# Performance work log

Measured on AMD Instinct MI355X. Metric: run time of the kernel, lower is better.

## Reference

```python
import jax, jax.numpy as jnp
import numpy as np
jax.config.update("jax_enable_x64", True)

T_OLD = 60000
T_NEW = 60000
NV = 30000
MAX_STEPS = 300
FB_CHUNK = 500  # T_OLD must be divisible by this

FACE_OPP = np.array([[1, 2, 3], [0, 2, 3], [0, 1, 3], [0, 1, 2]])
EDGES = [(0, 1), (0, 2), (0, 3), (1, 2), (1, 3), (2, 3)]


def setup_inputs() -> dict:
    key = jax.random.key(0)
    k1, k2, k3, k4, k5 = jax.random.split(key, 5)
    # distinct vertices per tet (sorted base + strictly increasing offsets)
    off = jnp.arange(4, dtype=jnp.int64)
    new_indices = jnp.sort(jax.random.randint(k1, (T_NEW, 4), 0, NV - 4, dtype=jnp.int64), axis=1) + off
    old_indices = jnp.sort(jax.random.randint(k2, (T_OLD, 4), 0, NV - 4, dtype=jnp.int64), axis=1) + off
    return {
        "new_indices": new_indices,
        "old_indices": old_indices,
        "old_cc": jax.random.normal(k3, (T_OLD, 3), dtype=jnp.float32),
        "new_cc": jax.random.normal(k4, (T_NEW, 3), dtype=jnp.float32),
        "vertex_positions": jax.random.uniform(k5, (NV, 3), dtype=jnp.float32),
    }


def _min_edge_length(verts, indices):
    p = verts[indices]  # (T,4,3)
    el = jnp.stack([jnp.linalg.norm(p[:, a] - p[:, b], axis=-1) for a, b in EDGES])
    return el.min(axis=0)


def _forward(new_indices, old_indices, old_cc, new_cc, vertex_positions):
    T_new = new_indices.shape[0]
    T_old = old_indices.shape[0]
    Vn = vertex_positions.shape[0]

    # --- 1. unchanged-tet detection via sorted-vertex int64 keys ---
    key4 = lambda s: ((s[:, 0] * Vn + s[:, 1]) * Vn + s[:, 2]) * Vn + s[:, 3]
    ok = key4(jnp.sort(old_indices, axis=1))
    nk = key4(jnp.sort(new_indices, axis=1))
    order = jnp.argsort(ok)
    sk = ok[order]
    pos = jnp.searchsorted(sk, nk, side='right') - 1
    posc = jnp.clip(pos, 0, T_old - 1)
    matched = jnp.where((pos >= 0) & (sk[posc] == nk), order[posc], -1)
    is_matched = matched >= 0
    matched_safe = jnp.maximum(matched, 0)

    # --- 2. face adjacency of old mesh (sorted face keys, adjacent-equal pairing) ---
    fi = jnp.sort(old_indices[:, FACE_OPP], axis=2)          # (T_old,4,3)
    fk = (fi[..., 0] * Vn + fi[..., 1]) * Vn + fi[..., 2]    # (T_old,4)
    all_keys = fk.T.reshape(-1)                              # f-major like the numpy concat
    all_tets = jnp.tile(jnp.arange(T_old), 4)
    all_locals = jnp.repeat(jnp.arange(4), T_old)
    o2 = jnp.argsort(all_keys)
    sk2, st, sl = all_keys[o2], all_tets[o2], all_locals[o2]
    same = sk2[:-1] == sk2[1:]
    neighbors = jnp.full((T_old, 4), -1, dtype=jnp.int64)
    neighbors = neighbors.at[jnp.where(same, st[:-1], T_old), sl[:-1]].set(st[1:], mode='drop')
    neighbors = neighbors.at[jnp.where(same, st[1:], T_old), sl[1:]].set(st[:-1], mode='drop')

    # --- 3. per-old-tet inverse edge matrix; degenerate tets get no neighbors ---
    verts = jax.lax.stop_gradient(vertex_positions).astype(jnp.float32)
    p = verts[old_indices]                                   # (T_old,4,3)
    v0 = p[:, 0]
    Tm = jnp.stack([p[:, 1] - v0, p[:, 2] - v0, p[:, 3] - v0], axis=-1)
    degen = jnp.abs(jnp.linalg.det(Tm)) < 1e-10
    Tinv = jnp.linalg.inv(jnp.where(degen[:, None, None], jnp.eye(3, dtype=Tm.dtype), Tm))
    neighbors = jnp.where(degen[:, None], -1, neighbors)

    prio = jnp.full((Vn,), -1, dtype=jnp.int64)
    ar = jnp.arange(T_old)
    for vi in range(4):
        prio = prio.at[old_indices[:, vi]].max(vi * T_old + ar)
    v2t = jnp.where(prio >= 0, prio % T_old, 0)

    # --- 5. barycentric walk (masked, all float inputs stop-gradiented; int outputs) ---
    cent = jax.lax.stop_gradient(verts[new_indices].mean(axis=1))  # (T_new,3)
    seed = v2t[new_indices[:, 0]]
    n_walk = jnp.sum(~is_matched)
    thr = jnp.maximum(jnp.int64(100), n_walk // 1000)

    def cond(state):
        step, cur, rem, act = state
        return (step < MAX_STEPS) & (jnp.sum(act) >= thr)

    def body(state):
        step, cur, rem, act = state
        rel = cent - v0[cur]
        bary = jnp.einsum('nij,nj->ni', Tinv[cur], rel)
        all_b = jnp.concatenate([(1.0 - bary.sum(axis=1))[:, None], bary], axis=1)
        conv = act & (all_b.min(axis=1) >= -1e-4)
        rem = jnp.where(conv, cur, rem)
        act = act & ~conv
        nb = neighbors[cur, jnp.argmin(all_b, axis=1)]
        at_bd = act & (nb < 0)
        rem = jnp.where(at_bd, cur, rem)
        act = act & ~at_bd
        cur = jnp.where(act, nb, cur)
        return (step + 1, cur, rem, act)

    _, cur, rem, act = jax.lax.while_loop(cond, body, (jnp.int64(0), seed, seed, ~is_matched))
    rem = jnp.where(act, cur, rem)

    # --- 6. nearest-centroid fallback for unfinished walks (gated, chunked) ---
    old_cents = jax.lax.stop_gradient(verts[old_indices].mean(axis=1))

    def fallback(_):
        p2 = (cent ** 2).sum(-1)
        c2 = (old_cents ** 2).sum(-1)
        def scan_body(carry, i):
            bd, bi = carry
            c = jax.lax.dynamic_slice(old_cents, (i * FB_CHUNK, 0), (FB_CHUNK, 3))
            cn = jax.lax.dynamic_slice(c2, (i * FB_CHUNK,), (FB_CHUNK,))
            d = p2[:, None] - 2.0 * (cent @ c.T) + cn[None, :]
            md = d.min(axis=1)
            mi = d.argmin(axis=1).astype(jnp.int64) + i * FB_CHUNK
            imp = md < bd
            return (jnp.where(imp, md, bd), jnp.where(imp, mi, bi)), None
        init = (jnp.full((T_new,), jnp.inf, dtype=jnp.float32), jnp.zeros((T_new,), dtype=jnp.int64))
        (bd, bi), _ = jax.lax.scan(scan_body, init, jnp.arange(T_old // FB_CHUNK))
        return bi

    fb = jax.lax.cond(jnp.sum(act) > 0, fallback, lambda _: jnp.zeros((T_new,), dtype=jnp.int64), None)
    rem = jnp.clip(jnp.where(act, fb, rem), 0, T_old - 1)
    remap = jnp.where(is_matched, matched_safe, rem)

    # --- 7. candidates: containing tet + 4 face neighbors ---
    face_nb = neighbors[remap]
    face_nb = jnp.where(face_nb >= 0, face_nb, remap[:, None])
    cands = jnp.concatenate([remap[:, None], face_nb], axis=1)            # (T_new,5)
    cands = jnp.where(is_matched[:, None], matched_safe[:, None], cands)

    # --- 8. overlap / circumcenter-distance weights ---
    cand_verts = old_indices[cands]                                       # (T_new,5,4)
    overlap = (cand_verts[:, :, :, None] == new_indices[:, None, None, :]).any(-1).sum(-1).astype(jnp.float32)
    cc_d2 = ((old_cc[cands] - new_cc[:, None, :]) ** 2).sum(-1)
    raw = jnp.exp(overlap * 2.0) / (cc_d2 + 1e-8)
    weights = raw / raw.sum(axis=1, keepdims=True)

    # --- 9. density scale: min-edge-length ratio ---
    old_el = _min_edge_length(vertex_positions, old_indices)[cands]
    new_el = _min_edge_length(vertex_positions, new_indices)
    density_scale = jnp.clip(old_el / jnp.maximum(new_el[:, None], 1e-8), 0.1, 10.0)

    return cands, weights, density_scale


_forward_jit = jax.jit(_forward)


def reference(new_indices, old_indices, old_cc, new_cc, vertex_positions):
    return _forward_jit(new_indices, old_indices, old_cc, new_cc, vertex_positions)
```

## Files before the change

kernel.cpp:

```cpp
#include <hip/hip_runtime.h>

#pragma clang fp contract(off)

#define TOLD 60000
#define TNEW 60000
#define NVERT 30000
#define MAXSTEPS 300
#define TKSZ 262144
#define TFBSZ 131072
#define FHSZ 131072
#define EMPTY64 0xFFFFFFFFFFFFFFFFULL
#define NWGR 60
#define VRANGE 500
#define NSLICE 16
#define TSLICE (TOLD / NSLICE)

#define NB_SETUP 235
#define NB_PRIO  (NWGR * NSLICE)
#define NB_INIT  187
#define NB_FACE  938
#define NB_FOLD  118
#define NB_WALK  235
#define NB_FB    120
#define FBRANGE  (TNEW / NB_FB)

#define OFF_FTAB     0u
#define OFF_TFB      1048576u
#define OFF_NBR      2097152u
#define FF_BYTES     3057152u
#define FF_UINT4     191072u
#define OFF_CNT      3057152u
#define OFF_TFV      3059200u
#define OFF_PPRIO    3583488u
#define OFF_PRIO     5503488u
#define OFF_IDXOLD   5623488u
#define OFF_SSTEP    6583488u
#define OFF_DEGEN    6823488u
#define OFF_TV4      7063488u
#define OFF_COLD4    9943488u
#define OFF_CNEW4    10903488u
#define OFF_TKEY2    11863488u
#define OFF_TVAL2    13960640u
#define OFF_DM       15009216u

struct P {
  const unsigned int* rawNew;
  const unsigned int* rawOld;
  const float* occ;
  const float* ncc;
  const float* verts;
  float* out;
  unsigned long long* tkey2;
  int* tval2;
  unsigned long long* tfb;
  int* tfv;
  unsigned long long* ftab;
  int* counters;
  int* idxOld;
  int* nbr;
  int* pprio;
  int* prio;
  int* sstep;
  int* degen;
  float4* Tv4;
  float4* cold4;
  float4* cnew4;
  unsigned long long* dm;
  unsigned int dmMask;
};

__device__ __forceinline__ unsigned hash64(unsigned long long k){
  k ^= k >> 33; k *= 0xff51afd7ed558ccdULL;
  k ^= k >> 33; k *= 0xc4ceb9fe1a85ec53ULL;
  k ^= k >> 33;
  return (unsigned)k;
}
__device__ __forceinline__ void cswap(int& a, int& b){ if (a > b){ int t = a; a = b; b = t; } }

__device__ __forceinline__ int detect64(const unsigned int* raw){
  unsigned acc = 0;
  const uint4* r4 = (const uint4*)raw;
  #pragma unroll
  for (int k = 0; k < 32; ++k){ uint4 v = r4[k]; acc |= (v.y | v.w); }
  return acc == 0u;
}

__device__ __forceinline__ int4 load_tet4(const unsigned int* raw, int is64, int t){
  if (is64){
    uint4 a = ((const uint4*)raw)[t * 2 + 0];
    uint4 b = ((const uint4*)raw)[t * 2 + 1];
    return make_int4((int)a.x, (int)a.z, (int)b.x, (int)b.z);
  }
  uint4 a = ((const uint4*)raw)[t];
  return make_int4((int)a.x, (int)a.y, (int)a.z, (int)a.w);
}

__device__ __forceinline__ void face_insert(unsigned long long* ftab, int* nbr,
                                            unsigned long long fkey, int t, int l){
  unsigned long long mine = (fkey << 18) | (unsigned long long)(t * 4 + l);
  unsigned slot = hash64(fkey ^ 0x9e3779b97f4a7c15ULL) & (FHSZ - 1);
  while (true){
    unsigned long long prev = atomicCAS(&ftab[slot], EMPTY64, mine);
    if (prev == EMPTY64) return;
    if ((prev >> 18) == fkey){
      int oid = (int)(prev & 0x3FFFFULL);
      nbr[t * 4 + l] = oid >> 2;
      nbr[oid] = t;
      return;
    }
    slot = (slot + 1) & (FHSZ - 1);
  }
}

__device__ __forceinline__ float min_edge_r(
    float q0x, float q0y, float q0z, float q1x, float q1y, float q1z,
    float q2x, float q2y, float q2z, float q3x, float q3y, float q3z){
  float m = 3.402823466e+38f;
  float dx, dy, dz, d;
  dx = q0x - q1x; dy = q0y - q1y; dz = q0z - q1z; d = sqrtf((dx*dx + dy*dy) + dz*dz); m = fminf(m, d);
  dx = q0x - q2x; dy = q0y - q2y; dz = q0z - q2z; d = sqrtf((dx*dx + dy*dy) + dz*dz); m = fminf(m, d);
  dx = q0x - q3x; dy = q0y - q3y; dz = q0z - q3z; d = sqrtf((dx*dx + dy*dy) + dz*dz); m = fminf(m, d);
  dx = q1x - q2x; dy = q1y - q2y; dz = q1z - q2z; d = sqrtf((dx*dx + dy*dy) + dz*dz); m = fminf(m, d);
  dx = q1x - q3x; dy = q1y - q3y; dz = q1z - q3z; d = sqrtf((dx*dx + dy*dy) + dz*dz); m = fminf(m, d);
  dx = q2x - q3x; dy = q2y - q3y; dz = q2z - q3z; d = sqrtf((dx*dx + dy*dy) + dz*dz); m = fminf(m, d);
  return m;
}

__global__ __launch_bounds__(256) void k_front(P p){
  __shared__ int sprio[VRANGE];
  int bb = blockIdx.x;
  if (bb < NB_SETUP){
    if (bb == 0){
      for (int j = threadIdx.x; j < 384; j += 256) p.counters[j] = 0;
    }
    int t = bb * 256 + threadIdx.x;
    if (t >= TOLD) return;
    int is64 = detect64(p.rawOld);
    int4 iv4 = load_tet4(p.rawOld, is64, t);
    int i0 = iv4.x, i1 = iv4.y, i2 = iv4.z, i3 = iv4.w;
    ((int4*)p.idxOld)[t] = iv4;

    {
      int s0 = i0, s1 = i1, s2 = i2, s3 = i3;
      cswap(s0, s1); cswap(s2, s3); cswap(s0, s2); cswap(s1, s3); cswap(s1, s2);
      unsigned long long key =
          (unsigned long long)((((long long)s0 * NVERT + s1) * NVERT + s2) * NVERT + s3);
      p.tkey2[hash64(key) & (TKSZ - 1)] = key;
    }

    if (p.dmMask){
      const int FO[4][3] = {{1, 2, 3}, {0, 2, 3}, {0, 1, 3}, {0, 1, 2}};
      int iv[4] = {i0, i1, i2, i3};
      #pragma unroll
      for (int l = 0; l < 4; ++l){
        int a = iv[FO[l][0]], b = iv[FO[l][1]], c = iv[FO[l][2]];
        cswap(a, b); cswap(a, c); cswap(b, c);
        unsigned long long fk = (unsigned long long)(((long long)a * NVERT + b) * NVERT + c);
        p.dm[hash64(fk) & p.dmMask] = (fk << 18) | (unsigned long long)(t * 4 + l);
      }
    }

    float q0x = p.verts[i0 * 3 + 0], q0y = p.verts[i0 * 3 + 1], q0z = p.verts[i0 * 3 + 2];
    float q1x = p.verts[i1 * 3 + 0], q1y = p.verts[i1 * 3 + 1], q1z = p.verts[i1 * 3 + 2];
    float q2x = p.verts[i2 * 3 + 0], q2y = p.verts[i2 * 3 + 1], q2z = p.verts[i2 * 3 + 2];
    float q3x = p.verts[i3 * 3 + 0], q3y = p.verts[i3 * 3 + 1], q3z = p.verts[i3 * 3 + 2];
    float e1x = q1x - q0x, e1y = q1y - q0y, e1z = q1z - q0z;
    float e2x = q2x - q0x, e2y = q2y - q0y, e2z = q2z - q0z;
    float e3x = q3x - q0x, e3y = q3y - q0y, e3z = q3z - q0z;
    float c23x = e2y * e3z - e2z * e3y;
    float c23y = e2z * e3x - e2x * e3z;
    float c23z = e2x * e3y - e2y * e3x;
    float det = e1x * c23x + e1y * c23y + e1z * c23z;
    int dg = (fabsf(det) < 1e-10f) ? 1 : 0;
    p.degen[t] = dg;
    float4 r0, r1, r2;
    if (dg){
      r0 = make_float4(1.f, 0.f, 0.f, q0x);
      r1 = make_float4(0.f, 1.f, 0.f, q0y);
      r2 = make_float4(0.f, 0.f, 1.f, q0z);
    } else {
      float inv = 1.0f / det;
      float c31x = e3y * e1z - e3z * e1y;
      float c31y = e3z * e1x - e3x * e1z;
      float c31z = e3x * e1y - e3y * e1x;
      float c12x = e1y * e2z - e1z * e2y;
      float c12y = e1z * e2x - e1x * e2z;
      float c12z = e1x * e2y - e1y * e2x;
      r0 = make_float4(c23x * inv, c23y * inv, c23z * inv, q0x);
      r1 = make_float4(c31x * inv, c31y * inv, c31z * inv, q0y);
      r2 = make_float4(c12x * inv, c12y * inv, c12z * inv, q0z);
    }
    p.Tv4[t * 3 + 0] = r0;
    p.Tv4[t * 3 + 1] = r1;
    p.Tv4[t * 3 + 2] = r2;
    float el = min_edge_r(q0x, q0y, q0z, q1x, q1y, q1z, q2x, q2y, q2z, q3x, q3y, q3z);
    p.cold4[t] = make_float4((((q0x + q1x) + q2x) + q3x) * 0.25f,
                             (((q0y + q1y) + q2y) + q3y) * 0.25f,
                             (((q0z + q1z) + q2z) + q3z) * 0.25f, el);
  } else if (bb < NB_SETUP + NB_PRIO){
    int rb = bb - NB_SETUP;
    int range = rb / NSLICE;
    int slice = rb % NSLICE;
    int base = range * VRANGE;
    for (int j = threadIdx.x; j < VRANGE; j += 256) sprio[j] = -1;
    __syncthreads();
    int is64 = detect64(p.rawOld);
    int t0 = slice * TSLICE;
    for (int t = t0 + threadIdx.x; t < t0 + TSLICE; t += 256){
      int4 iv = load_tet4(p.rawOld, is64, t);
      int v;
      v = iv.x - base; if ((unsigned)v < VRANGE) atomicMax(&sprio[v], 0 * TOLD + t);
      v = iv.y - base; if ((unsigned)v < VRANGE) atomicMax(&sprio[v], 1 * TOLD + t);
      v = iv.z - base; if ((unsigned)v < VRANGE) atomicMax(&sprio[v], 2 * TOLD + t);
      v = iv.w - base; if ((unsigned)v < VRANGE) atomicMax(&sprio[v], 3 * TOLD + t);
    }
    __syncthreads();
    for (int j = threadIdx.x; j < VRANGE; j += 256)
      p.pprio[slice * NVERT + base + j] = sprio[j];
  } else {
    unsigned idx = (unsigned)(bb - NB_SETUP - NB_PRIO) * 1024u + threadIdx.x * 4u;
    uint4 ff = make_uint4(~0u, ~0u, ~0u, ~0u);
    uint4* base = (uint4*)p.ftab;
    #pragma unroll
    for (unsigned k = 0; k < 4; ++k){
      unsigned id = idx + k;
      if (id < FF_UINT4) base[id] = ff;
    }
  }
}

__global__ __launch_bounds__(256) void k_mid(P p){
  int bb = blockIdx.x;
  if (bb < NB_FACE){
    int i = bb * 256 + threadIdx.x;
    if (i >= TOLD * 4) return;
    int t = i >> 2, l = i & 3;
    int4 iv4 = ((const int4*)p.idxOld)[t];
    int iv[4] = {iv4.x, iv4.y, iv4.z, iv4.w};

    if (l == 0){
      int s0 = iv4.x, s1 = iv4.y, s2 = iv4.z, s3 = iv4.w;
      cswap(s0, s1); cswap(s2, s3); cswap(s0, s2); cswap(s1, s3); cswap(s1, s2);
      unsigned long long key =
          (unsigned long long)((((long long)s0 * NVERT + s1) * NVERT + s2) * NVERT + s3);
      unsigned slot = hash64(key) & (TKSZ - 1);
      if (p.tkey2[slot] == key){
        p.tval2[slot] = t;
      } else {
        unsigned fs = hash64(key ^ 0x517cc1b727220a95ULL) & (TFBSZ - 1);
        while (true){
          unsigned long long prev = atomicCAS(&p.tfb[fs], EMPTY64, key);
          if (prev == EMPTY64){ p.tfv[fs] = t; break; }
          if (prev == key){ atomicMax(&p.tfv[fs], t); break; }
          fs = (fs + 1) & (TFBSZ - 1);
        }
      }
    }

    const int FO[4][3] = {{1, 2, 3}, {0, 2, 3}, {0, 1, 3}, {0, 1, 2}};
    int a = iv[FO[l][0]], b = iv[FO[l][1]], c = iv[FO[l][2]];
    cswap(a, b); cswap(a, c); cswap(b, c);
    unsigned long long fk = (unsigned long long)(((long long)a * NVERT + b) * NVERT + c);
    if (p.dmMask){
      unsigned long long mine = (fk << 18) | (unsigned long long)i;
      unsigned long long got = p.dm[hash64(fk) & p.dmMask];
      if (got == mine) return;
      if ((got >> 18) == fk){
        int wid = (int)(got & 0x3FFFFULL);
        p.nbr[i] = wid >> 2;
        p.nbr[wid] = t;
        return;
      }
    }
    face_insert(p.ftab, p.nbr, fk, t, l);
  } else {
    int v = (bb - NB_FACE) * 256 + threadIdx.x;
    if (v >= NVERT) return;
    int pr = -1;
    #pragma unroll
    for (int s = 0; s < NSLICE; ++s) pr = max(pr, p.pprio[s * NVERT + v]);
    p.prio[v] = pr;
  }
}

__device__ __forceinline__ void assemble_walker(const P& p, int n, int m, int remap,
                                                int4 ni, float nelv){
  int cds[5];
  if (m >= 0){
    cds[0] = cds[1] = cds[2] = cds[3] = cds[4] = m;
  } else {
    cds[0] = remap;
    int dg = p.degen[remap];
    int4 nb4 = ((const int4*)p.nbr)[remap];
    int nbl[4] = {nb4.x, nb4.y, nb4.z, nb4.w};
    for (int l = 0; l < 4; ++l){
      int fb = dg ? -1 : nbl[l];
      cds[1 + l] = (fb >= 0) ? fb : remap;
    }
  }
  bool same = (cds[1] == cds[0]) & (cds[2] == cds[0]) &
              (cds[3] == cds[0]) & (cds[4] == cds[0]);
  float nc0 = p.ncc[n * 3 + 0], nc1 = p.ncc[n * 3 + 1], nc2 = p.ncc[n * 3 + 2];
  if (same){
    int ct = cds[0];
    int4 cv = ((const int4*)p.idxOld)[ct];
    int ov = 0;
    ov += (cv.x == ni.x || cv.x == ni.y || cv.x == ni.z || cv.x == ni.w) ? 1 : 0;
    ov += (cv.y == ni.x || cv.y == ni.y || cv.y == ni.z || cv.y == ni.w) ? 1 : 0;
    ov += (cv.z == ni.x || cv.z == ni.y || cv.z == ni.z || cv.z == ni.w) ? 1 : 0;
    ov += (cv.w == ni.x || cv.w == ni.y || cv.w == ni.z || cv.w == ni.w) ? 1 : 0;
    float d0 = p.occ[ct * 3 + 0] - nc0;
    float d1 = p.occ[ct * 3 + 1] - nc1;
    float d2 = p.occ[ct * 3 + 2] - nc2;
    float ccd2 = (d0 * d0 + d1 * d1) + d2 * d2;
    float raw = expf((float)ov * 2.0f) / (ccd2 + 1e-8f);
    float rsum = 0.0f;
    rsum += raw; rsum += raw; rsum += raw; rsum += raw; rsum += raw;
    float wgt = raw / rsum;
    float ds = p.cold4[ct].w / nelv;
    ds = fminf(fmaxf(ds, 0.1f), 10.0f);
    float cf = (float)ct;
    for (int c = 0; c < 5; ++c){
      p.out[n * 5 + c] = cf;
      p.out[TNEW * 5 + n * 5 + c] = wgt;
      p.out[2 * TNEW * 5 + n * 5 + c] = ds;
    }
    return;
  }
  float raws[5]; float rsum = 0.0f;
  float oels[5];
  for (int c = 0; c < 5; ++c){
    int ct = cds[c];
    int4 cv = ((const int4*)p.idxOld)[ct];
    int ov = 0;
    ov += (cv.x == ni.x || cv.x == ni.y || cv.x == ni.z || cv.x == ni.w) ? 1 : 0;
    ov += (cv.y == ni.x || cv.y == ni.y || cv.y == ni.z || cv.y == ni.w) ? 1 : 0;
    ov += (cv.z == ni.x || cv.z == ni.y || cv.z == ni.z || cv.z == ni.w) ? 1 : 0;
    ov += (cv.w == ni.x || cv.w == ni.y || cv.w == ni.z || cv.w == ni.w) ? 1 : 0;
    float d0 = p.occ[ct * 3 + 0] - nc0;
    float d1 = p.occ[ct * 3 + 1] - nc1;
    float d2 = p.occ[ct * 3 + 2] - nc2;
    float ccd2 = (d0 * d0 + d1 * d1) + d2 * d2;
    float raw = expf((float)ov * 2.0f) / (ccd2 + 1e-8f);
    raws[c] = raw; rsum += raw;
    oels[c] = p.cold4[ct].w;
  }
  for (int c = 0; c < 5; ++c){
    p.out[n * 5 + c] = (float)cds[c];
    p.out[TNEW * 5 + n * 5 + c] = raws[c] / rsum;
    float ds = oels[c] / nelv;
    ds = fminf(fmaxf(ds, 0.1f), 10.0f);
    p.out[2 * TNEW * 5 + n * 5 + c] = ds;
  }
}

__global__ __launch_bounds__(256) void k_walkall(P p){
  __shared__ int s_hist[MAXSTEPS + 2];
  __shared__ int s_nw;
  for (int j = threadIdx.x; j < MAXSTEPS + 2; j += 256) s_hist[j] = 0;
  if (threadIdx.x == 0) s_nw = 0;
  __syncthreads();
  int n = blockIdx.x * blockDim.x + threadIdx.x;
  if (n < TNEW){
    int is64 = detect64(p.rawNew);
    int4 ni = load_tet4(p.rawNew, is64, n);

    float q0x = p.verts[ni.x * 3 + 0], q0y = p.verts[ni.x * 3 + 1], q0z = p.verts[ni.x * 3 + 2];
    float q1x = p.verts[ni.y * 3 + 0], q1y = p.verts[ni.y * 3 + 1], q1z = p.verts[ni.y * 3 + 2];
    float q2x = p.verts[ni.z * 3 + 0], q2y = p.verts[ni.z * 3 + 1], q2z = p.verts[ni.z * 3 + 2];
    float q3x = p.verts[ni.w * 3 + 0], q3y = p.verts[ni.w * 3 + 1], q3z = p.verts[ni.w * 3 + 2];
    float el = min_edge_r(q0x, q0y, q0z, q1x, q1y, q1z, q2x, q2y, q2z, q3x, q3y, q3z);
    float4 cn = make_float4((((q0x + q1x) + q2x) + q3x) * 0.25f,
                            (((q0y + q1y) + q2y) + q3y) * 0.25f,
                            (((q0z + q1z) + q2z) + q3z) * 0.25f, el);
    p.cnew4[n] = cn;
    float nelv = fmaxf(el, 1e-8f);

    int m = -1;
    {
      int s0 = ni.x, s1 = ni.y, s2 = ni.z, s3 = ni.w;
      cswap(s0, s1); cswap(s2, s3); cswap(s0, s2); cswap(s1, s3); cswap(s1, s2);
      unsigned long long key =
          (unsigned long long)((((long long)s0 * NVERT + s1) * NVERT + s2) * NVERT + s3);
      unsigned slot = hash64(key) & (TKSZ - 1);
      if (p.tkey2[slot] == key){
        m = p.tval2[slot];
      } else {
        unsigned fs = hash64(key ^ 0x517cc1b727220a95ULL) & (TFBSZ - 1);
        while (true){
          unsigned long long k2 = p.tfb[fs];
          if (k2 == EMPTY64) break;
          if (k2 == key){ m = p.tfv[fs]; break; }
          fs = (fs + 1) & (TFBSZ - 1);
        }
      }
    }
    if (m >= 0){
      p.sstep[n] = 0;
      assemble_walker(p, n, m, 0, ni, nelv);
    } else {
      atomicAdd(&s_nw, 1);
      int pr = p.prio[ni.x];
      int c = (pr >= 0) ? (pr % TOLD) : 0;
      int s = MAXSTEPS + 1;
      for (int k = 1; k <= MAXSTEPS; ++k){
        float4 r0 = p.Tv4[c * 3 + 0];
        float4 r1 = p.Tv4[c * 3 + 1];
        float4 r2 = p.Tv4[c * 3 + 2];
        float rx = cn.x - r0.w, ry = cn.y - r1.w, rz = cn.z - r2.w;
        float b0 = r0.x * rx + r0.y * ry + r0.z * rz;
        float b1 = r1.x * rx + r1.y * ry + r1.z * rz;
        float b2 = r2.x * rx + r2.y * ry + r2.z * rz;
        float a0 = 1.0f - (b0 + b1 + b2);
        float ab[4] = {a0, b0, b1, b2};
        int amin = 0; float mn = ab[0];
        for (int j = 1; j < 4; ++j){ if (ab[j] < mn){ mn = ab[j]; amin = j; } }
        if (mn >= -0.0001f){ s = k; break; }
        int nb = p.degen[c] ? -1 : p.nbr[c * 4 + amin];
        if (nb < 0){ s = k; break; }
        c = nb;
      }
      p.sstep[n] = s;
      atomicAdd(&s_hist[s], 1);
      assemble_walker(p, n, -1, c, ni, nelv);
    }
  }
  __syncthreads();
  if (threadIdx.x == 0 && s_nw) atomicAdd(&p.counters[0], s_nw);
  for (int j = threadIdx.x; j < MAXSTEPS + 2; j += 256){
    int v = s_hist[j];
    if (v) atomicAdd(&p.counters[64 + j], v);
  }
}

__device__ __forceinline__ int compute_S(const int* counters){
  int nw = counters[0];
  int thr = max(100, nw / 1000);
  if (nw < thr) return 0;
  int cnt = nw;
  for (int k = 1; k <= MAXSTEPS; ++k){
    cnt -= counters[64 + k];
    if (cnt < thr) return k;
  }
  return MAXSTEPS;
}

__global__ __launch_bounds__(256) void k_tail(P p){
  __shared__ float sd[256];
  __shared__ int si[256];
  __shared__ int s_hits[256];
  __shared__ int s_nhits;
  __shared__ int s_S;
  if (threadIdx.x == 0) s_S = compute_S(p.counters);
  __syncthreads();
  int S = s_S;
  int base = blockIdx.x * FBRANGE;
  for (int chunk = base; chunk < base + FBRANGE; chunk += 256){
    if (threadIdx.x == 0) s_nhits = 0;
    __syncthreads();
    int n = chunk + threadIdx.x;
    if (n < base + FBRANGE && n < TNEW){
      if (p.sstep[n] > S)
        s_hits[atomicAdd(&s_nhits, 1)] = n;
    }
    __syncthreads();
    int nh = s_nhits;
    for (int h = 0; h < nh; ++h){
      int n2 = s_hits[h];
      float4 cn = p.cnew4[n2];
      float cx = cn.x, cy = cn.y, cz = cn.z;
      float p2 = (cx * cx + cy * cy) + cz * cz;
      float bd = 3.402823466e+38f; int bi = 0;
      for (int j = threadIdx.x; j < TOLD; j += 256){
        float4 oc = p.cold4[j];
        float dot = (cx * oc.x + cy * oc.y) + cz * oc.z;
        float c2 = (oc.x * oc.x + oc.y * oc.y) + oc.z * oc.z;
        float d = (p2 - 2.0f * dot) + c2;
        if (d < bd || (d == bd && j < bi)){ bd = d; bi = j; }
      }
      sd[threadIdx.x] = bd; si[threadIdx.x] = bi;
      __syncthreads();
      for (int s = 128; s > 0; s >>= 1){
        if ((int)threadIdx.x < s){
          float od = sd[threadIdx.x + s]; int oi = si[threadIdx.x + s];
          if (od < sd[threadIdx.x] || (od == sd[threadIdx.x] && oi < si[threadIdx.x])){
            sd[threadIdx.x] = od; si[threadIdx.x] = oi;
          }
        }
        __syncthreads();
      }
      if (threadIdx.x == 0){
        int r = si[0];
        if (r < 0) r = 0; if (r > TOLD - 1) r = TOLD - 1;
        int is64 = detect64(p.rawNew);
        int4 ni = load_tet4(p.rawNew, is64, n2);
        float nelv = fmaxf(p.cnew4[n2].w, 1e-8f);
        assemble_walker(p, n2, -1, r, ni, nelv);
      }
      __syncthreads();
    }
    __syncthreads();
  }
}

extern "C" void kernel_launch(void* const* d_in, const int* in_sizes, int n_in,
                              void* d_out, int out_size, void* d_ws, size_t ws_size,
                              hipStream_t stream) {
  char* w = (char*)d_ws;
  P p;
  p.rawNew = (const unsigned int*)d_in[0];
  p.rawOld = (const unsigned int*)d_in[1];
  p.occ    = (const float*)d_in[2];
  p.ncc    = (const float*)d_in[3];
  p.verts  = (const float*)d_in[4];
  p.out    = (float*)d_out;
  p.ftab     = (unsigned long long*)(w + OFF_FTAB);
  p.tfb      = (unsigned long long*)(w + OFF_TFB);
  p.nbr      = (int*)(w + OFF_NBR);
  p.counters = (int*)(w + OFF_CNT);
  p.tfv      = (int*)(w + OFF_TFV);
  p.pprio    = (int*)(w + OFF_PPRIO);
  p.prio     = (int*)(w + OFF_PRIO);
  p.idxOld   = (int*)(w + OFF_IDXOLD);
  p.sstep    = (int*)(w + OFF_SSTEP);
  p.degen    = (int*)(w + OFF_DEGEN);
  p.Tv4      = (float4*)(w + OFF_TV4);
  p.cold4    = (float4*)(w + OFF_COLD4);
  p.cnew4    = (float4*)(w + OFF_CNEW4);
  p.tkey2    = (unsigned long long*)(w + OFF_TKEY2);
  p.tval2    = (int*)(w + OFF_TVAL2);
  p.dm       = (unsigned long long*)(w + OFF_DM);
  size_t avail = (ws_size > (size_t)OFF_DM) ? ws_size - (size_t)OFF_DM : 0;
  unsigned dmMask = 0;
  for (int bshift = 22; bshift >= 16; --bshift){
    if (avail >= ((size_t)8 << bshift)){ dmMask = (1u << bshift) - 1u; break; }
  }
  p.dmMask = dmMask;

  hipLaunchKernelGGL(k_front,   dim3(NB_SETUP + NB_PRIO + NB_INIT), dim3(256), 0, stream, p);
  hipLaunchKernelGGL(k_mid,     dim3(NB_FACE + NB_FOLD), dim3(256), 0, stream, p);
  hipLaunchKernelGGL(k_walkall, dim3(NB_WALK), dim3(256), 0, stream, p);
  hipLaunchKernelGGL(k_tail,    dim3(NB_FB), dim3(256), 0, stream, p);
}
```

Measured before the change: 109.5 us.

## Pack old/new tet records and precompute new-tet geometry in front kernel

Old tet indices, circumcenters and min edge length are packed into a single 32-byte record, so the candidate assembly needs two float4 loads instead of scattered occ/cold4/idxOld reads. New-tet centroid, min edge length and circumcenter are computed in extra blocks of the front kernel and stored as packed records. This removes the vertex gathers from the walk kernel's critical path. In exchange the front kernel does more work and the workspace grows.

```diff
diff --git a/kernel.cpp b/kernel.cpp
--- a/kernel.cpp
+++ b/kernel.cpp
@@ -16,6 +16,7 @@
 #define TSLICE (TOLD / NSLICE)
 
 #define NB_SETUP 235
+#define NB_NEWG  235
 #define NB_PRIO  (NWGR * NSLICE)
 #define NB_INIT  187
 #define NB_FACE  938
@@ -33,15 +34,15 @@
 #define OFF_TFV      3059200u
 #define OFF_PPRIO    3583488u
 #define OFF_PRIO     5503488u
-#define OFF_IDXOLD   5623488u
-#define OFF_SSTEP    6583488u
-#define OFF_DEGEN    6823488u
-#define OFF_TV4      7063488u
-#define OFF_COLD4    9943488u
-#define OFF_CNEW4    10903488u
-#define OFF_TKEY2    11863488u
-#define OFF_TVAL2    13960640u
-#define OFF_DM       15009216u
+#define OFF_OLDREC   5623488u
+#define OFF_SSTEP    7543488u
+#define OFF_DEGEN    7783488u
+#define OFF_TV4      8023488u
+#define OFF_COLD4    10903488u
+#define OFF_NEWREC   11863488u
+#define OFF_TKEY2    13783488u
+#define OFF_TVAL2    15880640u
+#define OFF_DM       16929216u
 
 struct P {
   const unsigned int* rawNew;
@@ -56,7 +57,8 @@
   int* tfv;
   unsigned long long* ftab;
   int* counters;
-  int* idxOld;
+  int4* oldrec;
+  float4* newrec;
   int* nbr;
   int* pprio;
   int* prio;
@@ -64,7 +66,6 @@
   int* degen;
   float4* Tv4;
   float4* cold4;
-  float4* cnew4;
   unsigned long long* dm;
   unsigned int dmMask;
 };
@@ -138,7 +139,6 @@
     int is64 = detect64(p.rawOld);
     int4 iv4 = load_tet4(p.rawOld, is64, t);
     int i0 = iv4.x, i1 = iv4.y, i2 = iv4.z, i3 = iv4.w;
-    ((int4*)p.idxOld)[t] = iv4;
 
     {
       int s0 = i0, s1 = i1, s2 = i2, s3 = i3;
@@ -197,8 +197,26 @@
     p.cold4[t] = make_float4((((q0x + q1x) + q2x) + q3x) * 0.25f,
                              (((q0y + q1y) + q2y) + q3y) * 0.25f,
                              (((q0z + q1z) + q2z) + q3z) * 0.25f, el);
-  } else if (bb < NB_SETUP + NB_PRIO){
-    int rb = bb - NB_SETUP;
+    p.oldrec[t * 2 + 0] = iv4;
+    ((float4*)p.oldrec)[t * 2 + 1] =
+        make_float4(p.occ[t * 3 + 0], p.occ[t * 3 + 1], p.occ[t * 3 + 2], el);
+  } else if (bb < NB_SETUP + NB_NEWG){
+    int n = (bb - NB_SETUP) * 256 + threadIdx.x;
+    if (n >= TNEW) return;
+    int is64 = detect64(p.rawNew);
+    int4 ni = load_tet4(p.rawNew, is64, n);
+    float q0x = p.verts[ni.x * 3 + 0], q0y = p.verts[ni.x * 3 + 1], q0z = p.verts[ni.x * 3 + 2];
+    float q1x = p.verts[ni.y * 3 + 0], q1y = p.verts[ni.y * 3 + 1], q1z = p.verts[ni.y * 3 + 2];
+    float q2x = p.verts[ni.z * 3 + 0], q2y = p.verts[ni.z * 3 + 1], q2z = p.verts[ni.z * 3 + 2];
+    float q3x = p.verts[ni.w * 3 + 0], q3y = p.verts[ni.w * 3 + 1], q3z = p.verts[ni.w * 3 + 2];
+    float el = min_edge_r(q0x, q0y, q0z, q1x, q1y, q1z, q2x, q2y, q2z, q3x, q3y, q3z);
+    p.newrec[n * 2 + 0] = make_float4((((q0x + q1x) + q2x) + q3x) * 0.25f,
+                                      (((q0y + q1y) + q2y) + q3y) * 0.25f,
+                                      (((q0z + q1z) + q2z) + q3z) * 0.25f, el);
+    p.newrec[n * 2 + 1] = make_float4(p.ncc[n * 3 + 0], p.ncc[n * 3 + 1],
+                                      p.ncc[n * 3 + 2], 0.0f);
+  } else if (bb < NB_SETUP + NB_NEWG + NB_PRIO){
+    int rb = bb - NB_SETUP - NB_NEWG;
     int range = rb / NSLICE;
     int slice = rb % NSLICE;
     int base = range * VRANGE;
@@ -218,7 +236,7 @@
     for (int j = threadIdx.x; j < VRANGE; j += 256)
       p.pprio[slice * NVERT + base + j] = sprio[j];
   } else {
-    unsigned idx = (unsigned)(bb - NB_SETUP - NB_PRIO) * 1024u + threadIdx.x * 4u;
+    unsigned idx = (unsigned)(bb - NB_SETUP - NB_NEWG - NB_PRIO) * 1024u + threadIdx.x * 4u;
     uint4 ff = make_uint4(~0u, ~0u, ~0u, ~0u);
     uint4* base = (uint4*)p.ftab;
     #pragma unroll
@@ -235,7 +253,7 @@
     int i = bb * 256 + threadIdx.x;
     if (i >= TOLD * 4) return;
     int t = i >> 2, l = i & 3;
-    int4 iv4 = ((const int4*)p.idxOld)[t];
+    int4 iv4 = p.oldrec[t * 2];
     int iv[4] = {iv4.x, iv4.y, iv4.z, iv4.w};
 
     if (l == 0){
@@ -284,7 +302,8 @@
 }
 
 __device__ __forceinline__ void assemble_walker(const P& p, int n, int m, int remap,
-                                                int4 ni, float nelv){
+                                                int4 ni, float nelv,
+                                                float nc0, float nc1, float nc2){
   int cds[5];
   if (m >= 0){
     cds[0] = cds[1] = cds[2] = cds[3] = cds[4] = m;
@@ -300,24 +319,24 @@
   }
   bool same = (cds[1] == cds[0]) & (cds[2] == cds[0]) &
               (cds[3] == cds[0]) & (cds[4] == cds[0]);
-  float nc0 = p.ncc[n * 3 + 0], nc1 = p.ncc[n * 3 + 1], nc2 = p.ncc[n * 3 + 2];
   if (same){
     int ct = cds[0];
-    int4 cv = ((const int4*)p.idxOld)[ct];
+    int4 cv = p.oldrec[ct * 2];
+    float4 of = ((const float4*)p.oldrec)[ct * 2 + 1];
     int ov = 0;
     ov += (cv.x == ni.x || cv.x == ni.y || cv.x == ni.z || cv.x == ni.w) ? 1 : 0;
     ov += (cv.y == ni.x || cv.y == ni.y || cv.y == ni.z || cv.y == ni.w) ? 1 : 0;
     ov += (cv.z == ni.x || cv.z == ni.y || cv.z == ni.z || cv.z == ni.w) ? 1 : 0;
     ov += (cv.w == ni.x || cv.w == ni.y || cv.w == ni.z || cv.w == ni.w) ? 1 : 0;
-    float d0 = p.occ[ct * 3 + 0] - nc0;
-    float d1 = p.occ[ct * 3 + 1] - nc1;
-    float d2 = p.occ[ct * 3 + 2] - nc2;
+    float d0 = of.x - nc0;
+    float d1 = of.y - nc1;
+    float d2 = of.z - nc2;
     float ccd2 = (d0 * d0 + d1 * d1) + d2 * d2;
     float raw = expf((float)ov * 2.0f) / (ccd2 + 1e-8f);
     float rsum = 0.0f;
     rsum += raw; rsum += raw; rsum += raw; rsum += raw; rsum += raw;
     float wgt = raw / rsum;
-    float ds = p.cold4[ct].w / nelv;
+    float ds = of.w / nelv;
     ds = fminf(fmaxf(ds, 0.1f), 10.0f);
     float cf = (float)ct;
     for (int c = 0; c < 5; ++c){
@@ -331,19 +350,20 @@
   float oels[5];
   for (int c = 0; c < 5; ++c){
     int ct = cds[c];
-    int4 cv = ((const int4*)p.idxOld)[ct];
+    int4 cv = p.oldrec[ct * 2];
+    float4 of = ((const float4*)p.oldrec)[ct * 2 + 1];
     int ov = 0;
     ov += (cv.x == ni.x || cv.x == ni.y || cv.x == ni.z || cv.x == ni.w) ? 1 : 0;
     ov += (cv.y == ni.x || cv.y == ni.y || cv.y == ni.z || cv.y == ni.w) ? 1 : 0;
     ov += (cv.z == ni.x || cv.z == ni.y || cv.z == ni.z || cv.z == ni.w) ? 1 : 0;
     ov += (cv.w == ni.x || cv.w == ni.y || cv.w == ni.z || cv.w == ni.w) ? 1 : 0;
-    float d0 = p.occ[ct * 3 + 0] - nc0;
-    float d1 = p.occ[ct * 3 + 1] - nc1;
-    float d2 = p.occ[ct * 3 + 2] - nc2;
+    float d0 = of.x - nc0;
+    float d1 = of.y - nc1;
+    float d2 = of.z - nc2;
     float ccd2 = (d0 * d0 + d1 * d1) + d2 * d2;
     float raw = expf((float)ov * 2.0f) / (ccd2 + 1e-8f);
     raws[c] = raw; rsum += raw;
-    oels[c] = p.cold4[ct].w;
+    oels[c] = of.w;
   }
   for (int c = 0; c < 5; ++c){
     p.out[n * 5 + c] = (float)cds[c];
@@ -364,17 +384,9 @@
   if (n < TNEW){
     int is64 = detect64(p.rawNew);
     int4 ni = load_tet4(p.rawNew, is64, n);
-
-    float q0x = p.verts[ni.x * 3 + 0], q0y = p.verts[ni.x * 3 + 1], q0z = p.verts[ni.x * 3 + 2];
-    float q1x = p.verts[ni.y * 3 + 0], q1y = p.verts[ni.y * 3 + 1], q1z = p.verts[ni.y * 3 + 2];
-    float q2x = p.verts[ni.z * 3 + 0], q2y = p.verts[ni.z * 3 + 1], q2z = p.verts[ni.z * 3 + 2];
-    float q3x = p.verts[ni.w * 3 + 0], q3y = p.verts[ni.w * 3 + 1], q3z = p.verts[ni.w * 3 + 2];
-    float el = min_edge_r(q0x, q0y, q0z, q1x, q1y, q1z, q2x, q2y, q2z, q3x, q3y, q3z);
-    float4 cn = make_float4((((q0x + q1x) + q2x) + q3x) * 0.25f,
-                            (((q0y + q1y) + q2y) + q3y) * 0.25f,
-                            (((q0z + q1z) + q2z) + q3z) * 0.25f, el);
-    p.cnew4[n] = cn;
-    float nelv = fmaxf(el, 1e-8f);
+    float4 na = p.newrec[n * 2 + 0];
+    float4 nb_ = p.newrec[n * 2 + 1];
+    float nelv = fmaxf(na.w, 1e-8f);
 
     int m = -1;
     {
@@ -397,7 +409,7 @@
     }
     if (m >= 0){
       p.sstep[n] = 0;
-      assemble_walker(p, n, m, 0, ni, nelv);
+      assemble_walker(p, n, m, 0, ni, nelv, nb_.x, nb_.y, nb_.z);
     } else {
       atomicAdd(&s_nw, 1);
       int pr = p.prio[ni.x];
@@ -407,7 +419,7 @@
         float4 r0 = p.Tv4[c * 3 + 0];
         float4 r1 = p.Tv4[c * 3 + 1];
         float4 r2 = p.Tv4[c * 3 + 2];
-        float rx = cn.x - r0.w, ry = cn.y - r1.w, rz = cn.z - r2.w;
+        float rx = na.x - r0.w, ry = na.y - r1.w, rz = na.z - r2.w;
         float b0 = r0.x * rx + r0.y * ry + r0.z * rz;
         float b1 = r1.x * rx + r1.y * ry + r1.z * rz;
         float b2 = r2.x * rx + r2.y * ry + r2.z * rz;
@@ -422,7 +434,7 @@
       }
       p.sstep[n] = s;
       atomicAdd(&s_hist[s], 1);
-      assemble_walker(p, n, -1, c, ni, nelv);
+      assemble_walker(p, n, -1, c, ni, nelv, nb_.x, nb_.y, nb_.z);
     }
   }
   __syncthreads();
@@ -467,7 +479,7 @@
     int nh = s_nhits;
     for (int h = 0; h < nh; ++h){
       int n2 = s_hits[h];
-      float4 cn = p.cnew4[n2];
+      float4 cn = p.newrec[n2 * 2 + 0];
       float cx = cn.x, cy = cn.y, cz = cn.z;
       float p2 = (cx * cx + cy * cy) + cz * cz;
       float bd = 3.402823466e+38f; int bi = 0;
@@ -494,8 +506,9 @@
         if (r < 0) r = 0; if (r > TOLD - 1) r = TOLD - 1;
         int is64 = detect64(p.rawNew);
         int4 ni = load_tet4(p.rawNew, is64, n2);
-        float nelv = fmaxf(p.cnew4[n2].w, 1e-8f);
-        assemble_walker(p, n2, -1, r, ni, nelv);
+        float4 nb_ = p.newrec[n2 * 2 + 1];
+        float nelv = fmaxf(cn.w, 1e-8f);
+        assemble_walker(p, n2, -1, r, ni, nelv, nb_.x, nb_.y, nb_.z);
       }
       __syncthreads();
     }
@@ -521,12 +534,12 @@
   p.tfv      = (int*)(w + OFF_TFV);
   p.pprio    = (int*)(w + OFF_PPRIO);
   p.prio     = (int*)(w + OFF_PRIO);
-  p.idxOld   = (int*)(w + OFF_IDXOLD);
+  p.oldrec   = (int4*)(w + OFF_OLDREC);
   p.sstep    = (int*)(w + OFF_SSTEP);
   p.degen    = (int*)(w + OFF_DEGEN);
   p.Tv4      = (float4*)(w + OFF_TV4);
   p.cold4    = (float4*)(w + OFF_COLD4);
-  p.cnew4    = (float4*)(w + OFF_CNEW4);
+  p.newrec   = (float4*)(w + OFF_NEWREC);
   p.tkey2    = (unsigned long long*)(w + OFF_TKEY2);
   p.tval2    = (int*)(w + OFF_TVAL2);
   p.dm       = (unsigned long long*)(w + OFF_DM);
@@ -537,7 +550,7 @@
   }
   p.dmMask = dmMask;
 
-  hipLaunchKernelGGL(k_front,   dim3(NB_SETUP + NB_PRIO + NB_INIT), dim3(256), 0, stream, p);
+  hipLaunchKernelGGL(k_front,   dim3(NB_SETUP + NB_NEWG + NB_PRIO + NB_INIT), dim3(256), 0, stream, p);
   hipLaunchKernelGGL(k_mid,     dim3(NB_FACE + NB_FOLD), dim3(256), 0, stream, p);
   hipLaunchKernelGGL(k_walkall, dim3(NB_WALK), dim3(256), 0, stream, p);
   hipLaunchKernelGGL(k_tail,    dim3(NB_FB), dim3(256), 0, stream, p);
```

Result: no change. 110.8 us (+1.2%).
